# Kernel optimization log

Hardware: AMD Instinct MI355X
Metric: run time of the kernel (lower is better)

## Reference

```python
import jax, jax.numpy as jnp
import numpy as np

B, H = 4096, 1024
N1, N2, N3 = 28, 280, 2800  # nodes (== classes == paths) per level, branching [28,10,10]


def setup_inputs() -> dict:
    key = jax.random.key(0)
    ks = jax.random.split(key, 8)
    s = 1.0 / np.sqrt(H)  # torch nn.Linear default init bound
    x = jax.random.normal(ks[0], (B, H), jnp.float32)
    labels = jax.random.randint(ks[1], (B,), 0, N3, dtype=jnp.int32)
    W1 = jax.random.uniform(ks[2], (N1, H), jnp.float32, -s, s)
    b1 = jax.random.uniform(ks[3], (N1,), jnp.float32, -s, s)
    W2 = jax.random.uniform(ks[4], (N2, H), jnp.float32, -s, s)
    b2 = jax.random.uniform(ks[5], (N2,), jnp.float32, -s, s)
    W3 = jax.random.uniform(ks[6], (N3, H), jnp.float32, -s, s)
    b3 = jax.random.uniform(ks[7], (N3,), jnp.float32, -s, s)
    return {"x": x, "labels": labels, "W1": W1, "b1": b1,
            "W2": W2, "b2": b2, "W3": W3, "b3": b3}


def _ce(logits, lab):
    # mean cross-entropy, same as torch.nn.CrossEntropyLoss (mean reduction)
    lp = jax.nn.log_softmax(logits, axis=-1)
    return -jnp.take_along_axis(lp, lab[:, None], axis=1).mean()


def reference(x, labels, W1, b1, W2, b2, W3, b3):
    # per-level node probabilities: one grouped GEMM per level replaces the
    # Python loop of tiny Linear(hidden,1)+sigmoid calls
    z1 = jax.nn.sigmoid(x @ W1.T + b1)  # [B, N1]
    z2 = jax.nn.sigmoid(x @ W2.T + b2)  # [B, N2]
    z3 = jax.nn.sigmoid(x @ W3.T + b3)  # [B, N3]

    # path (prefix) matrices: leaf k has path [k//100, k//10, k].
    # NOTE: all nodes of a path index into the CURRENT level's weights,
    # exactly as self.nodes[lvl][node] does in the source.
    i2 = jnp.arange(N2)
    p2 = jnp.stack([i2 // 10, i2], axis=1)                    # [N2, 2]
    i3 = jnp.arange(N3)
    p3 = jnp.stack([i3 // 100, i3 // 10, i3], axis=1)          # [N3, 3]

    logits1 = z1                                               # prod over length-1 path
    logits2 = jnp.prod(z2[:, p2], axis=-1)                     # [B, N2]
    logits3 = jnp.prod(z3[:, p3], axis=-1)                     # [B, N3]

    # update_label_per_lvl: label -> ancestor node id at that level
    lab1 = labels // 100
    lab2 = labels // 10
    loss = _ce(logits1, lab1) + _ce(logits2, lab2) + _ce(logits3, labels)
    return logits3, loss
```

## Files before the change

### kernel.cpp

```cpp
#include <hip/hip_runtime.h>
#include <cstdint>


typedef unsigned short u16;
typedef __bf16 bf16;
typedef bf16 bf16x8 __attribute__((ext_vector_type(8)));
typedef float f32x4 __attribute__((ext_vector_type(4)));

#define AS_G __attribute__((address_space(1)))
#define AS_L __attribute__((address_space(3)))

constexpr int BATCH = 4096;
constexpr int H     = 1024;
constexpr int N1 = 28, N2 = 280, N3 = 2800;
constexpr int NT = N1 + N2 + N3;
constexpr int NP = 3200;

__device__ inline u16 f2bf(float f) {
    unsigned int u = __float_as_uint(f);
    u += 0x7fffu + ((u >> 16) & 1u);
    return (u16)(u >> 16);
}

constexpr int XG = (BATCH * H) / 4;
constexpr int WG = (NP * H) / 4;
constexpr int BG = NP / 4;

__global__ __launch_bounds__(256) void cast_kernel(
        const float* __restrict__ x,
        const float* __restrict__ W1, const float* __restrict__ W2,
        const float* __restrict__ W3,
        const float* __restrict__ b1, const float* __restrict__ b2,
        const float* __restrict__ b3,
        u16* __restrict__ Xb, u16* __restrict__ Wb, float* __restrict__ biasf) {
    int g = blockIdx.x * 256 + threadIdx.x;
    if (g < XG) {
        float4 v = ((const float4*)x)[g];
        ((ushort4*)Xb)[g] = make_ushort4(f2bf(v.x), f2bf(v.y), f2bf(v.z), f2bf(v.w));
    } else if (g < XG + WG) {
        int wg = g - XG;
        int row = wg >> 8;
        int cg  = wg & 255;
        float4 v = make_float4(0.f, 0.f, 0.f, 0.f);
        if (row < N1)           v = ((const float4*)W1)[row * 256 + cg];
        else if (row < N1 + N2) v = ((const float4*)W2)[(row - N1) * 256 + cg];
        else if (row < NT)      v = ((const float4*)W3)[(row - N1 - N2) * 256 + cg];
        ((ushort4*)Wb)[wg] = make_ushort4(f2bf(v.x), f2bf(v.y), f2bf(v.z), f2bf(v.w));
    } else if (g < XG + WG + BG) {
        int bg = g - XG - WG;
        float4 v;
        float* vp = &v.x;
        #pragma unroll
        for (int i = 0; i < 4; ++i) {
            int c = bg * 4 + i;
            float t = 0.f;
            if (c < N1)           t = b1[c];
            else if (c < N1 + N2) t = b2[c - N1];
            else if (c < NT)      t = b3[c - N1 - N2];
            vp[i] = t;
        }
        ((float4*)biasf)[bg] = v;
    }
}

__global__ __launch_bounds__(256) void gemm_sig(
        const u16* __restrict__ Xb, const u16* __restrict__ Wb,
        const float* __restrict__ biasf, float* __restrict__ Z) {
    __shared__ __align__(16) u16 As[128 * 32];
    __shared__ __align__(16) u16 Bs[128 * 32];
    const int tid  = threadIdx.x;
    const int lane = tid & 63;
    const int wave = tid >> 6;
    const int m0 = blockIdx.y * 128;
    const int n0 = blockIdx.x * 128;
    const int wr = wave >> 1;
    const int wc = wave & 1;

    const int c0 = tid, c1 = tid + 256;
    const int r0 = c0 >> 2, o0 = (c0 & 3) * 8;
    const int r1 = c1 >> 2, o1 = (c1 & 3) * 8;

    const int laneM = lane & 15;
    const int laneK = (lane >> 4) * 8;

    f32x4 acc[4][4] = {};

    for (int kt = 0; kt < H / 32; ++kt) {
        const int k0 = kt * 32;
        __builtin_amdgcn_global_load_lds((const AS_G uint32_t*)(Xb + (size_t)(m0 + r0) * H + k0 + o0),
                                         (AS_L uint32_t*)&As[c0 * 8], 16, 0, 0);
        __builtin_amdgcn_global_load_lds((const AS_G uint32_t*)(Xb + (size_t)(m0 + r1) * H + k0 + o1),
                                         (AS_L uint32_t*)&As[c1 * 8], 16, 0, 0);
        __builtin_amdgcn_global_load_lds((const AS_G uint32_t*)(Wb + (size_t)(n0 + r0) * H + k0 + o0),
                                         (AS_L uint32_t*)&Bs[c0 * 8], 16, 0, 0);
        __builtin_amdgcn_global_load_lds((const AS_G uint32_t*)(Wb + (size_t)(n0 + r1) * H + k0 + o1),
                                         (AS_L uint32_t*)&Bs[c1 * 8], 16, 0, 0);
        __syncthreads();

        bf16x8 af[4], bfv[4];
        #pragma unroll
        for (int i = 0; i < 4; ++i) {
            af[i]  = *(const bf16x8*)&As[(wr * 64 + i * 16 + laneM) * 32 + laneK];
            bfv[i] = *(const bf16x8*)&Bs[(wc * 64 + i * 16 + laneM) * 32 + laneK];
        }
        #pragma unroll
        for (int am = 0; am < 4; ++am)
            #pragma unroll
            for (int bn = 0; bn < 4; ++bn)
                acc[am][bn] = __builtin_amdgcn_mfma_f32_16x16x32_bf16(af[am], bfv[bn], acc[am][bn], 0, 0, 0);
        __syncthreads();
    }

    #pragma unroll
    for (int bn = 0; bn < 4; ++bn) {
        const int col = n0 + wc * 64 + bn * 16 + laneM;
        if (col >= NT) continue;
        const float bias = biasf[col];
        #pragma unroll
        for (int am = 0; am < 4; ++am) {
            const int rbase = m0 + wr * 64 + am * 16 + (lane >> 4) * 4;
            #pragma unroll
            for (int r = 0; r < 4; ++r) {
                float v = acc[am][bn][r] + bias;
                Z[(size_t)(rbase + r) * NP + col] = 1.0f / (1.0f + __expf(-v));
            }
        }
    }
}

__global__ __launch_bounds__(256) void logits_loss(
        const float* __restrict__ Z, const int* __restrict__ labels,
        float* __restrict__ out, float* __restrict__ partials) {
    __shared__ float z1s[N1];
    __shared__ float z2s[N2];
    __shared__ float z3s[N3];
    __shared__ float red[12];
    const int b = blockIdx.x, tid = threadIdx.x;
    const float* Zr = Z + (size_t)b * NP;
    for (int i = tid; i < NT; i += 256) {
        float v = Zr[i];
        if (i < N1)           z1s[i] = v;
        else if (i < N1 + N2) z2s[i - N1] = v;
        else                  z3s[i - N1 - N2] = v;
    }
    __syncthreads();

    float se1 = 0.f, se2 = 0.f, se3 = 0.f;
    float* outr = out + (size_t)b * N3;
    for (int k = tid; k < N3; k += 256) {
        float lg = z3s[k] * z3s[k / 10] * z3s[k / 100];
        outr[k] = lg;
        se3 += expf(lg);
    }
    for (int j = tid; j < N2; j += 256)
        se2 += expf(z2s[j] * z2s[j / 10]);
    if (tid < N1)
        se1 = expf(z1s[tid]);

    #pragma unroll
    for (int off = 32; off > 0; off >>= 1) {
        se1 += __shfl_down(se1, off, 64);
        se2 += __shfl_down(se2, off, 64);
        se3 += __shfl_down(se3, off, 64);
    }
    if ((tid & 63) == 0) {
        int w = tid >> 6;
        red[w] = se3; red[4 + w] = se2; red[8 + w] = se1;
    }
    __syncthreads();
    if (tid == 0) {
        float s3 = red[0] + red[1] + red[2] + red[3];
        float s2 = red[4] + red[5] + red[6] + red[7];
        float s1 = red[8] + red[9] + red[10] + red[11];
        int lab  = labels[b];
        int lab2 = lab / 10, lab1 = lab / 100;
        float l1 = z1s[lab1];
        float l2 = z2s[lab2] * z2s[lab2 / 10];
        float l3 = z3s[lab] * z3s[lab2] * z3s[lab1];
        partials[b] = (logf(s1) - l1) + (logf(s2) - l2) + (logf(s3) - l3);
    }
}

__global__ __launch_bounds__(256) void final_reduce(
        const float* __restrict__ partials, float* __restrict__ out) {
    __shared__ float red[4];
    const int tid = threadIdx.x;
    float s = 0.f;
    for (int i = tid; i < BATCH; i += 256) s += partials[i];
    #pragma unroll
    for (int off = 32; off > 0; off >>= 1) s += __shfl_down(s, off, 64);
    if ((tid & 63) == 0) red[tid >> 6] = s;
    __syncthreads();
    if (tid == 0)
        out[(size_t)BATCH * N3] = (red[0] + red[1] + red[2] + red[3]) * (1.0f / BATCH);
}

extern "C" void kernel_launch(void* const* d_in, const int* in_sizes, int n_in,
                              void* d_out, int out_size, void* d_ws, size_t ws_size,
                              hipStream_t stream) {
    const float* x      = (const float*)d_in[0];
    const int*   labels = (const int*)d_in[1];
    const float* W1     = (const float*)d_in[2];
    const float* b1     = (const float*)d_in[3];
    const float* W2     = (const float*)d_in[4];
    const float* b2     = (const float*)d_in[5];
    const float* W3     = (const float*)d_in[6];
    const float* b3     = (const float*)d_in[7];
    float* out = (float*)d_out;

    char* ws = (char*)d_ws;
    u16*   Xb       = (u16*)ws;
    u16*   Wb       = (u16*)(ws + 8388608);
    float* Z        = (float*)(ws + 14942208);
    float* partials = (float*)(ws + 67371008);
    float* biasf    = (float*)(ws + 67387392);

    const int castGrid = (XG + WG + BG + 255) / 256;
    cast_kernel<<<castGrid, 256, 0, stream>>>(x, W1, W2, W3, b1, b2, b3, Xb, Wb, biasf);
    gemm_sig<<<dim3(NP / 128, BATCH / 128), 256, 0, stream>>>(Xb, Wb, biasf, Z);
    logits_loss<<<BATCH, 256, 0, stream>>>(Z, labels, out, partials);
    final_reduce<<<1, 256, 0, stream>>>(partials, out);
}
```

Baseline: 177.0 us.

## Double-buffer GEMM LDS, store sigmoid outputs as bf16, fold loss reduction into atomics

Double-buffers the LDS tiles in the GEMM so the next K-slice's global-to-LDS loads are issued before computing the current one. The sigmoid intermediate Z is stored as bf16 instead of fp32, halving the traffic between the GEMM and the logits kernel. The final reduction kernel is removed: each row atomically adds its scaled loss into the output slot, which the cast kernel zeroes. Costs are lower precision on logits, since a bf16-rounded z is multiplied three times, and atomic contention plus nondeterministic summation order for the loss.

```diff
diff --git a/kernel.cpp b/kernel.cpp
--- a/kernel.cpp
+++ b/kernel.cpp
@@ -20,6 +20,9 @@
     unsigned int u = __float_as_uint(f);
     u += 0x7fffu + ((u >> 16) & 1u);
     return (u16)(u >> 16);
+}
+__device__ inline float bf2f(unsigned int u) {
+    return __uint_as_float(u << 16);
 }
 
 constexpr int XG = (BATCH * H) / 4;
@@ -32,8 +35,10 @@
         const float* __restrict__ W3,
         const float* __restrict__ b1, const float* __restrict__ b2,
         const float* __restrict__ b3,
-        u16* __restrict__ Xb, u16* __restrict__ Wb, float* __restrict__ biasf) {
+        u16* __restrict__ Xb, u16* __restrict__ Wb, float* __restrict__ biasf,
+        float* __restrict__ loss_slot) {
     int g = blockIdx.x * 256 + threadIdx.x;
+    if (g == 0) loss_slot[0] = 0.f;
     if (g < XG) {
         float4 v = ((const float4*)x)[g];
         ((ushort4*)Xb)[g] = make_ushort4(f2bf(v.x), f2bf(v.y), f2bf(v.z), f2bf(v.w));
@@ -65,9 +70,9 @@
 
 __global__ __launch_bounds__(256) void gemm_sig(
         const u16* __restrict__ Xb, const u16* __restrict__ Wb,
-        const float* __restrict__ biasf, float* __restrict__ Z) {
-    __shared__ __align__(16) u16 As[128 * 32];
-    __shared__ __align__(16) u16 Bs[128 * 32];
+        const float* __restrict__ biasf, u16* __restrict__ Zb) {
+    __shared__ __align__(16) u16 As[2][128 * 32];
+    __shared__ __align__(16) u16 Bs[2][128 * 32];
     const int tid  = threadIdx.x;
     const int lane = tid & 63;
     const int wave = tid >> 6;
@@ -85,31 +90,52 @@
 
     f32x4 acc[4][4] = {};
 
-    for (int kt = 0; kt < H / 32; ++kt) {
-        const int k0 = kt * 32;
-        __builtin_amdgcn_global_load_lds((const AS_G uint32_t*)(Xb + (size_t)(m0 + r0) * H + k0 + o0),
-                                         (AS_L uint32_t*)&As[c0 * 8], 16, 0, 0);
-        __builtin_amdgcn_global_load_lds((const AS_G uint32_t*)(Xb + (size_t)(m0 + r1) * H + k0 + o1),
-                                         (AS_L uint32_t*)&As[c1 * 8], 16, 0, 0);
-        __builtin_amdgcn_global_load_lds((const AS_G uint32_t*)(Wb + (size_t)(n0 + r0) * H + k0 + o0),
-                                         (AS_L uint32_t*)&Bs[c0 * 8], 16, 0, 0);
-        __builtin_amdgcn_global_load_lds((const AS_G uint32_t*)(Wb + (size_t)(n0 + r1) * H + k0 + o1),
-                                         (AS_L uint32_t*)&Bs[c1 * 8], 16, 0, 0);
+    const u16* gA0 = Xb + (size_t)(m0 + r0) * H + o0;
+    const u16* gA1 = Xb + (size_t)(m0 + r1) * H + o1;
+    const u16* gB0 = Wb + (size_t)(n0 + r0) * H + o0;
+    const u16* gB1 = Wb + (size_t)(n0 + r1) * H + o1;
+
+#define STAGE(buf, kt)                                                                     \
+    do {                                                                                   \
+        const int kk = (kt) * 32;                                                          \
+        __builtin_amdgcn_global_load_lds((const AS_G uint32_t*)(gA0 + kk),                 \
+                                         (AS_L uint32_t*)&As[buf][c0 * 8], 16, 0, 0);      \
+        __builtin_amdgcn_global_load_lds((const AS_G uint32_t*)(gA1 + kk),                 \
+                                         (AS_L uint32_t*)&As[buf][c1 * 8], 16, 0, 0);      \
+        __builtin_amdgcn_global_load_lds((const AS_G uint32_t*)(gB0 + kk),                 \
+                                         (AS_L uint32_t*)&Bs[buf][c0 * 8], 16, 0, 0);      \
+        __builtin_amdgcn_global_load_lds((const AS_G uint32_t*)(gB1 + kk),                 \
+                                         (AS_L uint32_t*)&Bs[buf][c1 * 8], 16, 0, 0);      \
+    } while (0)
+
+#define COMPUTE(buf)                                                                       \
+    do {                                                                                   \
+        bf16x8 af[4], bfv[4];                                                              \
+        _Pragma("unroll")                                                                  \
+        for (int i = 0; i < 4; ++i) {                                                      \
+            af[i]  = *(const bf16x8*)&As[buf][(wr * 64 + i * 16 + laneM) * 32 + laneK];    \
+            bfv[i] = *(const bf16x8*)&Bs[buf][(wc * 64 + i * 16 + laneM) * 32 + laneK];    \
+        }                                                                                  \
+        _Pragma("unroll")                                                                  \
+        for (int am = 0; am < 4; ++am)                                                     \
+            _Pragma("unroll")                                                              \
+            for (int bn = 0; bn < 4; ++bn)                                                 \
+                acc[am][bn] = __builtin_amdgcn_mfma_f32_16x16x32_bf16(af[am], bfv[bn],     \
+                                                                      acc[am][bn], 0, 0, 0); \
+    } while (0)
+
+    STAGE(0, 0);
+    __syncthreads();
+    for (int kt = 0; kt < H / 32; kt += 2) {
+        STAGE(1, kt + 1);
+        COMPUTE(0);
         __syncthreads();
-
-        bf16x8 af[4], bfv[4];
-        #pragma unroll
-        for (int i = 0; i < 4; ++i) {
-            af[i]  = *(const bf16x8*)&As[(wr * 64 + i * 16 + laneM) * 32 + laneK];
-            bfv[i] = *(const bf16x8*)&Bs[(wc * 64 + i * 16 + laneM) * 32 + laneK];
-        }
-        #pragma unroll
-        for (int am = 0; am < 4; ++am)
-            #pragma unroll
-            for (int bn = 0; bn < 4; ++bn)
-                acc[am][bn] = __builtin_amdgcn_mfma_f32_16x16x32_bf16(af[am], bfv[bn], acc[am][bn], 0, 0, 0);
+        if (kt + 2 < H / 32) STAGE(0, kt + 2);
+        COMPUTE(1);
         __syncthreads();
     }
+#undef STAGE
+#undef COMPUTE
 
     #pragma unroll
     for (int bn = 0; bn < 4; ++bn) {
@@ -122,28 +148,30 @@
             #pragma unroll
             for (int r = 0; r < 4; ++r) {
                 float v = acc[am][bn][r] + bias;
-                Z[(size_t)(rbase + r) * NP + col] = 1.0f / (1.0f + __expf(-v));
+                Zb[(size_t)(rbase + r) * NP + col] = f2bf(1.0f / (1.0f + __expf(-v)));
             }
         }
     }
 }
 
 __global__ __launch_bounds__(256) void logits_loss(
-        const float* __restrict__ Z, const int* __restrict__ labels,
-        float* __restrict__ out, float* __restrict__ partials) {
-    __shared__ float z1s[N1];
-    __shared__ float z2s[N2];
-    __shared__ float z3s[N3];
+        const u16* __restrict__ Zb, const int* __restrict__ labels,
+        float* __restrict__ out, float* __restrict__ loss_slot) {
+    __shared__ float zs[NT];
     __shared__ float red[12];
     const int b = blockIdx.x, tid = threadIdx.x;
-    const float* Zr = Z + (size_t)b * NP;
-    for (int i = tid; i < NT; i += 256) {
-        float v = Zr[i];
-        if (i < N1)           z1s[i] = v;
-        else if (i < N1 + N2) z2s[i - N1] = v;
-        else                  z3s[i - N1 - N2] = v;
+
+    const unsigned int* Zr = (const unsigned int*)(Zb + (size_t)b * NP);
+    for (int i = tid; i < NT / 2; i += 256) {
+        unsigned int v = Zr[i];
+        zs[2 * i]     = bf2f(v & 0xffffu);
+        zs[2 * i + 1] = bf2f(v >> 16);
     }
     __syncthreads();
+
+    const float* z1s = zs;
+    const float* z2s = zs + N1;
+    const float* z3s = zs + N1 + N2;
 
     float se1 = 0.f, se2 = 0.f, se3 = 0.f;
     float* outr = out + (size_t)b * N3;
@@ -177,22 +205,9 @@
         float l1 = z1s[lab1];
         float l2 = z2s[lab2] * z2s[lab2 / 10];
         float l3 = z3s[lab] * z3s[lab2] * z3s[lab1];
-        partials[b] = (logf(s1) - l1) + (logf(s2) - l2) + (logf(s3) - l3);
-    }
-}
-
-__global__ __launch_bounds__(256) void final_reduce(
-        const float* __restrict__ partials, float* __restrict__ out) {
-    __shared__ float red[4];
-    const int tid = threadIdx.x;
-    float s = 0.f;
-    for (int i = tid; i < BATCH; i += 256) s += partials[i];
-    #pragma unroll
-    for (int off = 32; off > 0; off >>= 1) s += __shfl_down(s, off, 64);
-    if ((tid & 63) == 0) red[tid >> 6] = s;
-    __syncthreads();
-    if (tid == 0)
-        out[(size_t)BATCH * N3] = (red[0] + red[1] + red[2] + red[3]) * (1.0f / BATCH);
+        float loss = (logf(s1) - l1) + (logf(s2) - l2) + (logf(s3) - l3);
+        atomicAdd(loss_slot, loss * (1.0f / BATCH));
+    }
 }
 
 extern "C" void kernel_launch(void* const* d_in, const int* in_sizes, int n_in,
@@ -207,17 +222,16 @@
     const float* W3     = (const float*)d_in[6];
     const float* b3     = (const float*)d_in[7];
     float* out = (float*)d_out;
+    float* loss_slot = out + (size_t)BATCH * N3;
 
     char* ws = (char*)d_ws;
-    u16*   Xb       = (u16*)ws;
-    u16*   Wb       = (u16*)(ws + 8388608);
-    float* Z        = (float*)(ws + 14942208);
-    float* partials = (float*)(ws + 67371008);
-    float* biasf    = (float*)(ws + 67387392);
+    u16*   Xb    = (u16*)ws;
+    u16*   Wb    = (u16*)(ws + 8388608);
+    u16*   Zb    = (u16*)(ws + 14942208);
+    float* biasf = (float*)(ws + 41156608);
 
     const int castGrid = (XG + WG + BG + 255) / 256;
-    cast_kernel<<<castGrid, 256, 0, stream>>>(x, W1, W2, W3, b1, b2, b3, Xb, Wb, biasf);
-    gemm_sig<<<dim3(NP / 128, BATCH / 128), 256, 0, stream>>>(Xb, Wb, biasf, Z);
-    logits_loss<<<BATCH, 256, 0, stream>>>(Z, labels, out, partials);
-    final_reduce<<<1, 256, 0, stream>>>(partials, out);
-}
+    cast_kernel<<<castGrid, 256, 0, stream>>>(x, W1, W2, W3, b1, b2, b3, Xb, Wb, biasf, loss_slot);
+    gemm_sig<<<dim3(NP / 128, BATCH / 128), 256, 0, stream>>>(Xb, Wb, biasf, Zb);
+    logits_loss<<<BATCH, 256, 0, stream>>>(Zb, labels, out, loss_slot);
+}
```

Result: slower. 212.4 us (+20.0%).

## Store sigmoid output as bf16, swizzle GEMM blocks per XCD, fuse loss reduction

Applied to the files above, without the earlier changes.

The GEMM epilogue now writes the sigmoid activations as bf16 rather than fp32, which halves the traffic for the intermediate Z buffer. The GEMM grid becomes a 1-D launch remapped so that each XCD works on a contiguous band of rows, aiming for better L2 reuse of X tiles. The logits kernel unpacks bf16 pairs, writes its output as float4, and uses fast __expf. The separate final-reduce kernel is replaced by an atomicAdd into the loss slot, which the cast kernel zeroes first. The cost is lower precision in the output logits and a loss sum whose order is no longer deterministic.

```diff
diff --git a/kernel.cpp b/kernel.cpp
--- a/kernel.cpp
+++ b/kernel.cpp
@@ -21,6 +21,7 @@
     u += 0x7fffu + ((u >> 16) & 1u);
     return (u16)(u >> 16);
 }
+__device__ inline float bf2f(unsigned int u) { return __uint_as_float(u << 16); }
 
 constexpr int XG = (BATCH * H) / 4;
 constexpr int WG = (NP * H) / 4;
@@ -32,15 +33,16 @@
         const float* __restrict__ W3,
         const float* __restrict__ b1, const float* __restrict__ b2,
         const float* __restrict__ b3,
-        u16* __restrict__ Xb, u16* __restrict__ Wb, float* __restrict__ biasf) {
+        u16* __restrict__ Xb, u16* __restrict__ Wb, float* __restrict__ biasf,
+        float* __restrict__ loss_slot) {
     int g = blockIdx.x * 256 + threadIdx.x;
+    if (g == 0) loss_slot[0] = 0.f;
     if (g < XG) {
         float4 v = ((const float4*)x)[g];
         ((ushort4*)Xb)[g] = make_ushort4(f2bf(v.x), f2bf(v.y), f2bf(v.z), f2bf(v.w));
     } else if (g < XG + WG) {
         int wg = g - XG;
-        int row = wg >> 8;
-        int cg  = wg & 255;
+        int row = wg >> 8, cg = wg & 255;
         float4 v = make_float4(0.f, 0.f, 0.f, 0.f);
         if (row < N1)           v = ((const float4*)W1)[row * 256 + cg];
         else if (row < N1 + N2) v = ((const float4*)W2)[(row - N1) * 256 + cg];
@@ -48,12 +50,10 @@
         ((ushort4*)Wb)[wg] = make_ushort4(f2bf(v.x), f2bf(v.y), f2bf(v.z), f2bf(v.w));
     } else if (g < XG + WG + BG) {
         int bg = g - XG - WG;
-        float4 v;
-        float* vp = &v.x;
+        float4 v; float* vp = &v.x;
         #pragma unroll
         for (int i = 0; i < 4; ++i) {
-            int c = bg * 4 + i;
-            float t = 0.f;
+            int c = bg * 4 + i; float t = 0.f;
             if (c < N1)           t = b1[c];
             else if (c < N1 + N2) t = b2[c - N1];
             else if (c < NT)      t = b3[c - N1 - N2];
@@ -65,14 +65,19 @@
 
 __global__ __launch_bounds__(256) void gemm_sig(
         const u16* __restrict__ Xb, const u16* __restrict__ Wb,
-        const float* __restrict__ biasf, float* __restrict__ Z) {
+        const float* __restrict__ biasf, u16* __restrict__ Zb) {
     __shared__ __align__(16) u16 As[128 * 32];
     __shared__ __align__(16) u16 Bs[128 * 32];
+
+    const int id  = blockIdx.x;
+    const int xcd = id & 7;
+    const int j   = id >> 3;
+    const int m0 = ((xcd << 2) | (j & 3)) * 128;
+    const int n0 = (j >> 2) * 128;
+
     const int tid  = threadIdx.x;
     const int lane = tid & 63;
     const int wave = tid >> 6;
-    const int m0 = blockIdx.y * 128;
-    const int n0 = blockIdx.x * 128;
     const int wr = wave >> 1;
     const int wc = wave & 1;
 
@@ -122,40 +127,50 @@
             #pragma unroll
             for (int r = 0; r < 4; ++r) {
                 float v = acc[am][bn][r] + bias;
-                Z[(size_t)(rbase + r) * NP + col] = 1.0f / (1.0f + __expf(-v));
+                Zb[(size_t)(rbase + r) * NP + col] = f2bf(1.0f / (1.0f + __expf(-v)));
             }
         }
     }
 }
 
 __global__ __launch_bounds__(256) void logits_loss(
-        const float* __restrict__ Z, const int* __restrict__ labels,
-        float* __restrict__ out, float* __restrict__ partials) {
-    __shared__ float z1s[N1];
-    __shared__ float z2s[N2];
-    __shared__ float z3s[N3];
+        const u16* __restrict__ Zb, const int* __restrict__ labels,
+        float* __restrict__ out, float* __restrict__ loss_slot) {
+    __shared__ float zs[NT];
     __shared__ float red[12];
     const int b = blockIdx.x, tid = threadIdx.x;
-    const float* Zr = Z + (size_t)b * NP;
-    for (int i = tid; i < NT; i += 256) {
-        float v = Zr[i];
-        if (i < N1)           z1s[i] = v;
-        else if (i < N1 + N2) z2s[i - N1] = v;
-        else                  z3s[i - N1 - N2] = v;
+
+    const unsigned int* Zr = (const unsigned int*)(Zb + (size_t)b * NP);
+    for (int i = tid; i < NT / 2; i += 256) {
+        unsigned int v = Zr[i];
+        zs[2 * i]     = bf2f(v & 0xffffu);
+        zs[2 * i + 1] = bf2f(v >> 16);
     }
     __syncthreads();
 
+    const float* z1s = zs;
+    const float* z2s = zs + N1;
+    const float* z3s = zs + N1 + N2;
+
     float se1 = 0.f, se2 = 0.f, se3 = 0.f;
-    float* outr = out + (size_t)b * N3;
-    for (int k = tid; k < N3; k += 256) {
-        float lg = z3s[k] * z3s[k / 10] * z3s[k / 100];
-        outr[k] = lg;
-        se3 += expf(lg);
-    }
-    for (int j = tid; j < N2; j += 256)
-        se2 += expf(z2s[j] * z2s[j / 10]);
+    float4* outr4 = (float4*)(out + (size_t)b * N3);
+    for (int q = tid; q < N3 / 4; q += 256) {
+        const int k = q * 4;
+        float4 o;
+        float* op = &o.x;
+        #pragma unroll
+        for (int u = 0; u < 4; ++u) {
+            const int kk = k + u;
+            float lg = z3s[kk] * z3s[kk / 10] * z3s[kk / 100];
+            op[u] = lg;
+            se3 += __expf(lg);
+        }
+        outr4[q] = o;
+    }
+    for (int jj = tid; jj < N2; jj += 256)
+        se2 += __expf(z2s[jj] * z2s[jj / 10]);
     if (tid < N1)
-        se1 = expf(z1s[tid]);
+        se1 = __expf(z1s[tid]);
 
     #pragma unroll
     for (int off = 32; off > 0; off >>= 1) {
@@ -177,22 +192,9 @@
         float l1 = z1s[lab1];
         float l2 = z2s[lab2] * z2s[lab2 / 10];
         float l3 = z3s[lab] * z3s[lab2] * z3s[lab1];
-        partials[b] = (logf(s1) - l1) + (logf(s2) - l2) + (logf(s3) - l3);
-    }
-}
-
-__global__ __launch_bounds__(256) void final_reduce(
-        const float* __restrict__ partials, float* __restrict__ out) {
-    __shared__ float red[4];
-    const int tid = threadIdx.x;
-    float s = 0.f;
-    for (int i = tid; i < BATCH; i += 256) s += partials[i];
-    #pragma unroll
-    for (int off = 32; off > 0; off >>= 1) s += __shfl_down(s, off, 64);
-    if ((tid & 63) == 0) red[tid >> 6] = s;
-    __syncthreads();
-    if (tid == 0)
-        out[(size_t)BATCH * N3] = (red[0] + red[1] + red[2] + red[3]) * (1.0f / BATCH);
+        float loss = (logf(s1) - l1) + (logf(s2) - l2) + (logf(s3) - l3);
+        atomicAdd(loss_slot, loss * (1.0f / BATCH));
+    }
 }
 
 extern "C" void kernel_launch(void* const* d_in, const int* in_sizes, int n_in,
@@ -207,17 +209,16 @@
     const float* W3     = (const float*)d_in[6];
     const float* b3     = (const float*)d_in[7];
     float* out = (float*)d_out;
+    float* loss_slot = out + (size_t)BATCH * N3;
 
     char* ws = (char*)d_ws;
-    u16*   Xb       = (u16*)ws;
-    u16*   Wb       = (u16*)(ws + 8388608);
-    float* Z        = (float*)(ws + 14942208);
-    float* partials = (float*)(ws + 67371008);
-    float* biasf    = (float*)(ws + 67387392);
-
-    const int castGrid = (XG + WG + BG + 255) / 256;
-    cast_kernel<<<castGrid, 256, 0, stream>>>(x, W1, W2, W3, b1, b2, b3, Xb, Wb, biasf);
-    gemm_sig<<<dim3(NP / 128, BATCH / 128), 256, 0, stream>>>(Xb, Wb, biasf, Z);
-    logits_loss<<<BATCH, 256, 0, stream>>>(Z, labels, out, partials);
-    final_reduce<<<1, 256, 0, stream>>>(partials, out);
-}
+    u16*   Xb    = (u16*)ws;
+    u16*   Wb    = (u16*)(ws + 8388608);
+    u16*   Zb    = (u16*)(ws + 14942208);
+    float* biasf = (float*)(ws + 41156608);
+
+    cast_kernel<<<(XG + WG + BG + 255) / 256, 256, 0, stream>>>(
+        x, W1, W2, W3, b1, b2, b3, Xb, Wb, biasf, loss_slot);
+    gemm_sig<<<800, 256, 0, stream>>>(Xb, Wb, biasf, Zb);
+    logits_loss<<<BATCH, 256, 0, stream>>>(Zb, labels, out, loss_slot);
+}
```

Measured after the change: 205.3 us. 16.0% more time.
